# Optimization experiments

Measured on AMD Instinct MI355X. Metric: run time of the kernel, lower is better.

## Reference

```python
import jax, jax.numpy as jnp
import numpy as np


def setup_inputs() -> dict:
    key = jax.random.key(0)
    k1, k2, k3, k4 = jax.random.split(key, 4)
    B, S, I, O = 2, 4096, 4096, 4096
    x = jax.random.normal(k1, (B, S, I), dtype=jnp.float32)
    # packed int4 weights: each byte holds two nibbles; [O, I//2]
    qweight = jax.random.randint(k2, (O, I // 2), 0, 256, dtype=jnp.int32)
    # per-tensor weight scale (scalar, stored as shape [1])
    weight_scale = jax.random.uniform(k3, (1,), dtype=jnp.float32) * 0.01 + 1e-3
    bias = jax.random.normal(k4, (O,), dtype=jnp.float32)
    return {"x": x, "qweight": qweight, "weight_scale": weight_scale, "bias": bias}


def _dequant_weight(qweight, weight_scale):
    # unpack_int4 (dim=1): high nibble -> even cols, low nibble -> odd cols
    high = (qweight >> 4) - 8           # [O, I//2], values in [-8, 7]
    low = (qweight & 15) - 8            # [O, I//2]
    unpacked = jnp.stack([high, low], axis=-1).reshape(qweight.shape[0], -1)  # [O, I]
    # no weight_offset -> w = q * scale
    return unpacked.astype(weight_scale.dtype) * weight_scale


def reference(x, qweight, weight_scale, bias):
    w = _dequant_weight(qweight, weight_scale)  # [O, I] fp32
    # dynamic per-tensor symmetric int8 activation quantization
    max_abs = jnp.max(jnp.abs(x))
    scale = max_abs / 127.0
    scale = jnp.where(scale == 0, jnp.ones_like(scale), scale)
    x_dq = jnp.round(x / scale) * scale  # fake-quantized activations (offset = 0)
    # F.linear: x @ w.T + bias
    out = jnp.einsum('bsi,oi->bso', x_dq, w) + bias
    return out.astype(x.dtype)
```

## Files before the change

### kernel.cpp

```cpp
#include <hip/hip_runtime.h>


typedef __attribute__((ext_vector_type(4))) int int32x4;

__device__ __forceinline__ void async_copy16(const void* gsrc, void* ldsdst) {
  __builtin_amdgcn_global_load_lds(
      (const __attribute__((address_space(1))) void*)gsrc,
      (__attribute__((address_space(3))) void*)ldsdst, 16, 0, 0);
}

__global__ void amax_kernel(const float* __restrict__ x,
                            float* __restrict__ partial, int n4) {
  int tid = blockIdx.x * blockDim.x + threadIdx.x;
  int stride = gridDim.x * blockDim.x;
  float m = 0.0f;
  const float4* x4 = (const float4*)x;
  for (int i = tid; i < n4; i += stride) {
    float4 v = x4[i];
    m = fmaxf(m, fmaxf(fmaxf(fabsf(v.x), fabsf(v.y)),
                       fmaxf(fabsf(v.z), fabsf(v.w))));
  }
#pragma unroll
  for (int off = 32; off > 0; off >>= 1)
    m = fmaxf(m, __shfl_down(m, off, 64));
  __shared__ float red[4];
  if ((threadIdx.x & 63) == 0) red[threadIdx.x >> 6] = m;
  __syncthreads();
  if (threadIdx.x == 0) {
    partial[blockIdx.x] = fmaxf(fmaxf(red[0], red[1]), fmaxf(red[2], red[3]));
  }
}

__global__ void quant_kernel(const float* __restrict__ x,
                             const float* __restrict__ partial,
                             float* __restrict__ amax_out,
                             unsigned* __restrict__ qx, int n4) {
  const int t = threadIdx.x;
  float m = fmaxf(partial[t], partial[t + 256]);
#pragma unroll
  for (int off = 32; off > 0; off >>= 1)
    m = fmaxf(m, __shfl_down(m, off, 64));
  __shared__ float red[4];
  if ((t & 63) == 0) red[t >> 6] = m;
  __syncthreads();
  __shared__ float s_bcast;
  if (t == 0) {
    float amax = fmaxf(fmaxf(red[0], red[1]), fmaxf(red[2], red[3]));
    if (blockIdx.x == 0) *amax_out = amax;
    float s = amax / 127.0f;
    if (s == 0.0f) s = 1.0f;
    s_bcast = 1.0f / s;
  }
  __syncthreads();
  const float inv = s_bcast;

  int tid = blockIdx.x * blockDim.x + t;
  int stride = gridDim.x * blockDim.x;
  const float4* x4 = (const float4*)x;
  for (int i = tid; i < n4; i += stride) {
    float4 v = x4[i];
    int a = __float2int_rn(v.x * inv);
    int b = __float2int_rn(v.y * inv);
    int c = __float2int_rn(v.z * inv);
    int d = __float2int_rn(v.w * inv);
    qx[i] = (unsigned)(a & 0xFF) | ((unsigned)(b & 0xFF) << 8) |
            ((unsigned)(c & 0xFF) << 16) | ((unsigned)(d & 0xFF) << 24);
  }
}

__device__ __forceinline__ unsigned pack2(int q) {
  unsigned hi = (unsigned)((((q >> 4) & 15) - 8) & 0xFF);
  unsigned lo = (unsigned)(((q & 15) - 8) & 0xFF);
  return hi | (lo << 8);
}

__global__ void repack_kernel(const int* __restrict__ qw,
                              uint2* __restrict__ w8, int n4) {
  int tid = blockIdx.x * blockDim.x + threadIdx.x;
  int stride = gridDim.x * blockDim.x;
  const int4* q4 = (const int4*)qw;
  for (int i = tid; i < n4; i += stride) {
    int4 q = q4[i];
    uint2 r;
    r.x = pack2(q.x) | (pack2(q.y) << 16);
    r.y = pack2(q.z) | (pack2(q.w) << 16);
    w8[i] = r;
  }
}

#define BM 256
#define BN 256
#define BKT 64
#define TILE_B (BM * BKT)

#define TILE_BODY(t, CUR_AL, CUR_BF, NXT_AL, NXT_BF)                          \
  {                                                                           \
    const char* Ab = &As[((t) & 3) * TILE_B];                                 \
     \
    _Pragma("unroll") for (int i = 0; i < 4; ++i) afH[i] =                    \
        *(const int32x4*)(Ab + (arow0 + 64 + i * 16) * BKT + xsl);            \
    if ((t) + 3 < NT) {                                                       \
      const char* sa = aS + ((t) + 3) * BKT;                                  \
      char* ad = aD + (((t) + 3) & 3) * TILE_B;                               \
      async_copy16(sa, ad);                                                   \
      async_copy16(sa + skip, ad + 8192);                                     \
    }                                                                         \
     \
    asm volatile("s_waitcnt lgkmcnt(4)" ::: "memory");                        \
    __builtin_amdgcn_s_setprio(1);                                            \
    _Pragma("unroll") for (int i = 0; i < 4; ++i)                             \
        _Pragma("unroll") for (int j = 0; j < 4; ++j) acc[i][j] =             \
            __builtin_amdgcn_mfma_i32_16x16x64_i8(CUR_AL[i], CUR_BF[j],       \
                                                  acc[i][j], 0, 0, 0);        \
    __builtin_amdgcn_s_setprio(0);                                            \
           \
    if ((t) + 1 < NT) {                                                       \
           \
      asm volatile("s_waitcnt lgkmcnt(0)" ::: "memory");                      \
        \
      if ((t) + 4 <= NT)                                                      \
        asm volatile("s_waitcnt vmcnt(6)" ::: "memory");                      \
      else if ((t) + 3 <= NT)                                                 \
        asm volatile("s_waitcnt vmcnt(4)" ::: "memory");                      \
      else                                                                    \
        asm volatile("s_waitcnt vmcnt(0)" ::: "memory");                      \
      __builtin_amdgcn_s_barrier();                                           \
      __builtin_amdgcn_sched_barrier(0);    \
      const char* Abn = &As[(((t) + 1) & 3) * TILE_B];                        \
      const char* Bbn = &Bs[(((t) + 1) & 3) * TILE_B];                        \
      _Pragma("unroll") for (int i = 0; i < 4; ++i) NXT_AL[i] =               \
          *(const int32x4*)(Abn + (arow0 + i * 16) * BKT + xsl);              \
      _Pragma("unroll") for (int j = 0; j < 4; ++j) NXT_BF[j] =               \
          *(const int32x4*)(Bbn + (brow0 + j * 16) * BKT + xsl);              \
    }                                                                         \
    if ((t) + 3 < NT) {                                                       \
      const char* sb = bS + ((t) + 3) * BKT;                                  \
      char* bd = bD + (((t) + 3) & 3) * TILE_B;                               \
      async_copy16(sb, bd);                                                   \
      async_copy16(sb + skip, bd + 8192);                                     \
    }                                                                         \
    __builtin_amdgcn_s_setprio(1);                                            \
    _Pragma("unroll") for (int i = 0; i < 4; ++i)                             \
        _Pragma("unroll") for (int j = 0; j < 4; ++j) acc[4 + i][j] =         \
            __builtin_amdgcn_mfma_i32_16x16x64_i8(afH[i], CUR_BF[j],          \
                                                  acc[4 + i][j], 0, 0, 0);    \
    __builtin_amdgcn_s_setprio(0);                                            \
  }

__global__ __launch_bounds__(512, 2) void gemm_i8(
    const char* __restrict__ A, const char* __restrict__ Bt,
    const float* __restrict__ bias, const float* __restrict__ amax_p,
    const float* __restrict__ wscale, float* __restrict__ C,
    int M, int N, int K) {
  __shared__ alignas(16) char As[4 * TILE_B];
  __shared__ alignas(16) char Bs[4 * TILE_B];

  const int tid = threadIdx.x;
  const int lane = tid & 63;
  const int wave = tid >> 6;
  const int wm = wave >> 2;
  const int wn = wave & 3;
  const int quad = lane >> 4;
  const int l16 = lane & 15;

  const int cpx = gridDim.x >> 3;
  const int wg = (blockIdx.x & 7) * cpx + (blockIdx.x >> 3);
  const int bM = (wg >> 4) * BM;
  const int bN = (wg & 15) * BN;

  const int NT = K >> 6;

  const int srow = tid >> 2;
  const int scoff = (((tid & 3) ^ ((tid >> 3) & 3)) << 4);
  const char* aS = A + (size_t)(bM + srow) * K + scoff;
  const char* bS = Bt + (size_t)(bN + srow) * K + scoff;
  const size_t skip = (size_t)128 * K;
  char* aD = &As[tid * 16];
  char* bD = &Bs[tid * 16];

  for (int tt = 0; tt < 3; ++tt) {
    const int boff = tt * TILE_B;
    const char* sa = aS + tt * BKT;
    const char* sb = bS + tt * BKT;
    async_copy16(sa, aD + boff);
    async_copy16(sa + skip, aD + boff + 8192);
    async_copy16(sb, bD + boff);
    async_copy16(sb + skip, bD + boff + 8192);
  }

  const int xsl = ((quad ^ ((l16 >> 1) & 3)) << 4);
  const int arow0 = (wm << 7) + l16;
  const int brow0 = (wn << 6) + l16;

  int32x4 acc[8][4] = {};
  int32x4 afL0[4], bf0[4], afL1[4], bf1[4], afH[4];

  asm volatile("s_waitcnt vmcnt(8)" ::: "memory");
  __builtin_amdgcn_s_barrier();
  __builtin_amdgcn_sched_barrier(0);

#pragma unroll
  for (int i = 0; i < 4; ++i)
    afL0[i] = *(const int32x4*)(&As[0] + (arow0 + i * 16) * BKT + xsl);
#pragma unroll
  for (int j = 0; j < 4; ++j)
    bf0[j] = *(const int32x4*)(&Bs[0] + (brow0 + j * 16) * BKT + xsl);

  for (int t = 0; t < NT; t += 2) {
    TILE_BODY(t, afL0, bf0, afL1, bf1);
    TILE_BODY(t + 1, afL1, bf1, afL0, bf0);
  }

  float s = *amax_p / 127.0f;
  if (s == 0.0f) s = 1.0f;
  const float cs = s * wscale[0];

#pragma unroll
  for (int f = 0; f < 8; ++f) {
#pragma unroll
    for (int j = 0; j < 4; ++j) {
      const int n = bN + (wn << 6) + j * 16 + l16;
#pragma unroll
      for (int r = 0; r < 4; ++r) {
        const int m = bM + (wm << 7) + f * 16 + quad * 4 + r;
        C[(size_t)m * N + n] = (float)acc[f][j][r] * cs + bias[n];
      }
    }
  }
}

extern "C" void kernel_launch(void* const* d_in, const int* in_sizes, int n_in,
                              void* d_out, int out_size, void* d_ws,
                              size_t ws_size, hipStream_t stream) {
  const float* x = (const float*)d_in[0];
  const int* qw = (const int*)d_in[1];
  const float* wscale = (const float*)d_in[2];
  const float* bias = (const float*)d_in[3];
  float* out = (float*)d_out;

  const int nx = in_sizes[0];
  const int npacked = in_sizes[1];
  const int O = in_sizes[3];
  const int I = (npacked / O) * 2;
  const int M = nx / I;

  float* amax = (float*)d_ws;
  float* partial = (float*)((char*)d_ws + 256);
  char* qx = (char*)d_ws + 8192;
  char* w8 = qx + (size_t)nx;

  amax_kernel<<<512, 256, 0, stream>>>(x, partial, nx / 4);
  quant_kernel<<<2048, 256, 0, stream>>>(x, partial, amax, (unsigned*)qx,
                                         nx / 4);
  repack_kernel<<<1024, 256, 0, stream>>>(qw, (uint2*)w8, npacked / 4);

  const int nwg = (M / BM) * (O / BN);
  gemm_i8<<<nwg, 512, 0, stream>>>(qx, w8, bias, amax, wscale, out, M, O, I);
}
```

Before: 397.1 us.

## Use 4-wave GEMM workgroups with 128x128 per-wave tiles and widen amax reduction

The int8 GEMM workgroup drops from 8 waves to 4, and each wave now computes a 128x128 output tile (8x8 MFMA fragments) instead of 128x64. Each thread issues four async global-to-LDS copies per operand per stage instead of two, and the vmcnt thresholds are adjusted to match. The aim is more register-level reuse of A/B fragments per LDS read. The cost is a large jump in accumulator VGPR usage (256 accumulator registers), one workgroup per CU, and less latency hiding. Separately, the amax kernel gets twice as many blocks, each loop iteration loads two float4s, and the quant kernel reduces over 1024 partials.

```diff
diff --git a/kernel.cpp b/kernel.cpp
--- a/kernel.cpp
+++ b/kernel.cpp
@@ -15,10 +15,14 @@
   int stride = gridDim.x * blockDim.x;
   float m = 0.0f;
   const float4* x4 = (const float4*)x;
-  for (int i = tid; i < n4; i += stride) {
+  for (int i = tid; i < n4; i += 2 * stride) {
     float4 v = x4[i];
+    float4 w = (i + stride < n4) ? x4[i + stride]
+                                 : make_float4(0.f, 0.f, 0.f, 0.f);
     m = fmaxf(m, fmaxf(fmaxf(fabsf(v.x), fabsf(v.y)),
                        fmaxf(fabsf(v.z), fabsf(v.w))));
+    m = fmaxf(m, fmaxf(fmaxf(fabsf(w.x), fabsf(w.y)),
+                       fmaxf(fabsf(w.z), fabsf(w.w))));
   }
 #pragma unroll
   for (int off = 32; off > 0; off >>= 1)
@@ -36,7 +40,8 @@
                              float* __restrict__ amax_out,
                              unsigned* __restrict__ qx, int n4) {
   const int t = threadIdx.x;
-  float m = fmaxf(partial[t], partial[t + 256]);
+  float m = fmaxf(fmaxf(partial[t], partial[t + 256]),
+                  fmaxf(partial[t + 512], partial[t + 768]));
 #pragma unroll
   for (int off = 32; off > 0; off >>= 1)
     m = fmaxf(m, __shfl_down(m, off, 64));
@@ -96,32 +101,33 @@
 #define TILE_BODY(t, CUR_AL, CUR_BF, NXT_AL, NXT_BF)                          \
   {                                                                           \
     const char* Ab = &As[((t) & 3) * TILE_B];                                 \
-     \
+       \
     _Pragma("unroll") for (int i = 0; i < 4; ++i) afH[i] =                    \
         *(const int32x4*)(Ab + (arow0 + 64 + i * 16) * BKT + xsl);            \
     if ((t) + 3 < NT) {                                                       \
       const char* sa = aS + ((t) + 3) * BKT;                                  \
       char* ad = aD + (((t) + 3) & 3) * TILE_B;                               \
       async_copy16(sa, ad);                                                   \
-      async_copy16(sa + skip, ad + 8192);                                     \
+      async_copy16(sa + skip1, ad + 4096);                                    \
+      async_copy16(sa + skip2, ad + 8192);                                    \
+      async_copy16(sa + skip3, ad + 12288);                                   \
     }                                                                         \
-     \
+          \
     asm volatile("s_waitcnt lgkmcnt(4)" ::: "memory");                        \
     __builtin_amdgcn_s_setprio(1);                                            \
     _Pragma("unroll") for (int i = 0; i < 4; ++i)                             \
-        _Pragma("unroll") for (int j = 0; j < 4; ++j) acc[i][j] =             \
+        _Pragma("unroll") for (int j = 0; j < 8; ++j) acc[i][j] =             \
             __builtin_amdgcn_mfma_i32_16x16x64_i8(CUR_AL[i], CUR_BF[j],       \
                                                   acc[i][j], 0, 0, 0);        \
     __builtin_amdgcn_s_setprio(0);                                            \
            \
     if ((t) + 1 < NT) {                                                       \
-           \
       asm volatile("s_waitcnt lgkmcnt(0)" ::: "memory");                      \
-        \
+                   \
       if ((t) + 4 <= NT)                                                      \
-        asm volatile("s_waitcnt vmcnt(6)" ::: "memory");                      \
+        asm volatile("s_waitcnt vmcnt(12)" ::: "memory");                     \
       else if ((t) + 3 <= NT)                                                 \
-        asm volatile("s_waitcnt vmcnt(4)" ::: "memory");                      \
+        asm volatile("s_waitcnt vmcnt(8)" ::: "memory");                      \
       else                                                                    \
         asm volatile("s_waitcnt vmcnt(0)" ::: "memory");                      \
       __builtin_amdgcn_s_barrier();                                           \
@@ -130,24 +136,26 @@
       const char* Bbn = &Bs[(((t) + 1) & 3) * TILE_B];                        \
       _Pragma("unroll") for (int i = 0; i < 4; ++i) NXT_AL[i] =               \
           *(const int32x4*)(Abn + (arow0 + i * 16) * BKT + xsl);              \
-      _Pragma("unroll") for (int j = 0; j < 4; ++j) NXT_BF[j] =               \
+      _Pragma("unroll") for (int j = 0; j < 8; ++j) NXT_BF[j] =               \
           *(const int32x4*)(Bbn + (brow0 + j * 16) * BKT + xsl);              \
     }                                                                         \
     if ((t) + 3 < NT) {                                                       \
       const char* sb = bS + ((t) + 3) * BKT;                                  \
       char* bd = bD + (((t) + 3) & 3) * TILE_B;                               \
       async_copy16(sb, bd);                                                   \
-      async_copy16(sb + skip, bd + 8192);                                     \
+      async_copy16(sb + skip1, bd + 4096);                                    \
+      async_copy16(sb + skip2, bd + 8192);                                    \
+      async_copy16(sb + skip3, bd + 12288);                                   \
     }                                                                         \
     __builtin_amdgcn_s_setprio(1);                                            \
     _Pragma("unroll") for (int i = 0; i < 4; ++i)                             \
-        _Pragma("unroll") for (int j = 0; j < 4; ++j) acc[4 + i][j] =         \
+        _Pragma("unroll") for (int j = 0; j < 8; ++j) acc[4 + i][j] =         \
             __builtin_amdgcn_mfma_i32_16x16x64_i8(afH[i], CUR_BF[j],          \
                                                   acc[4 + i][j], 0, 0, 0);    \
     __builtin_amdgcn_s_setprio(0);                                            \
   }
 
-__global__ __launch_bounds__(512, 2) void gemm_i8(
+__global__ __launch_bounds__(256, 1) void gemm_i8(
     const char* __restrict__ A, const char* __restrict__ Bt,
     const float* __restrict__ bias, const float* __restrict__ amax_p,
     const float* __restrict__ wscale, float* __restrict__ C,
@@ -158,8 +166,8 @@
   const int tid = threadIdx.x;
   const int lane = tid & 63;
   const int wave = tid >> 6;
-  const int wm = wave >> 2;
-  const int wn = wave & 3;
+  const int wm = wave >> 1;
+  const int wn = wave & 1;
   const int quad = lane >> 4;
   const int l16 = lane & 15;
 
@@ -174,7 +182,9 @@
   const int scoff = (((tid & 3) ^ ((tid >> 3) & 3)) << 4);
   const char* aS = A + (size_t)(bM + srow) * K + scoff;
   const char* bS = Bt + (size_t)(bN + srow) * K + scoff;
-  const size_t skip = (size_t)128 * K;
+  const size_t skip1 = (size_t)64 * K;
+  const size_t skip2 = (size_t)128 * K;
+  const size_t skip3 = (size_t)192 * K;
   char* aD = &As[tid * 16];
   char* bD = &Bs[tid * 16];
 
@@ -183,19 +193,24 @@
     const char* sa = aS + tt * BKT;
     const char* sb = bS + tt * BKT;
     async_copy16(sa, aD + boff);
-    async_copy16(sa + skip, aD + boff + 8192);
+    async_copy16(sa + skip1, aD + boff + 4096);
+    async_copy16(sa + skip2, aD + boff + 8192);
+    async_copy16(sa + skip3, aD + boff + 12288);
     async_copy16(sb, bD + boff);
-    async_copy16(sb + skip, bD + boff + 8192);
+    async_copy16(sb + skip1, bD + boff + 4096);
+    async_copy16(sb + skip2, bD + boff + 8192);
+    async_copy16(sb + skip3, bD + boff + 12288);
   }
 
   const int xsl = ((quad ^ ((l16 >> 1) & 3)) << 4);
   const int arow0 = (wm << 7) + l16;
-  const int brow0 = (wn << 6) + l16;
-
-  int32x4 acc[8][4] = {};
-  int32x4 afL0[4], bf0[4], afL1[4], bf1[4], afH[4];
-
-  asm volatile("s_waitcnt vmcnt(8)" ::: "memory");
+  const int brow0 = (wn << 7) + l16;
+
+  int32x4 acc[8][8] = {};
+  int32x4 afL0[4], afL1[4], afH[4];
+  int32x4 bf0[8], bf1[8];
+
+  asm volatile("s_waitcnt vmcnt(16)" ::: "memory");
   __builtin_amdgcn_s_barrier();
   __builtin_amdgcn_sched_barrier(0);
 
@@ -203,7 +218,7 @@
   for (int i = 0; i < 4; ++i)
     afL0[i] = *(const int32x4*)(&As[0] + (arow0 + i * 16) * BKT + xsl);
 #pragma unroll
-  for (int j = 0; j < 4; ++j)
+  for (int j = 0; j < 8; ++j)
     bf0[j] = *(const int32x4*)(&Bs[0] + (brow0 + j * 16) * BKT + xsl);
 
   for (int t = 0; t < NT; t += 2) {
@@ -216,14 +231,14 @@
   const float cs = s * wscale[0];
 
 #pragma unroll
-  for (int f = 0; f < 8; ++f) {
-#pragma unroll
-    for (int j = 0; j < 4; ++j) {
-      const int n = bN + (wn << 6) + j * 16 + l16;
+  for (int fi = 0; fi < 8; ++fi) {
+#pragma unroll
+    for (int fj = 0; fj < 8; ++fj) {
+      const int n = bN + (wn << 7) + fj * 16 + l16;
 #pragma unroll
       for (int r = 0; r < 4; ++r) {
-        const int m = bM + (wm << 7) + f * 16 + quad * 4 + r;
-        C[(size_t)m * N + n] = (float)acc[f][j][r] * cs + bias[n];
+        const int m = bM + (wm << 7) + fi * 16 + quad * 4 + r;
+        C[(size_t)m * N + n] = (float)acc[fi][fj][r] * cs + bias[n];
       }
     }
   }
@@ -249,11 +264,11 @@
   char* qx = (char*)d_ws + 8192;
   char* w8 = qx + (size_t)nx;
 
-  amax_kernel<<<512, 256, 0, stream>>>(x, partial, nx / 4);
+  amax_kernel<<<1024, 256, 0, stream>>>(x, partial, nx / 4);
   quant_kernel<<<2048, 256, 0, stream>>>(x, partial, amax, (unsigned*)qx,
                                          nx / 4);
   repack_kernel<<<1024, 256, 0, stream>>>(qw, (uint2*)w8, npacked / 4);
 
   const int nwg = (M / BM) * (O / BN);
-  gemm_i8<<<nwg, 512, 0, stream>>>(qx, w8, bias, amax, wscale, out, M, O, I);
-}
+  gemm_i8<<<nwg, 256, 0, stream>>>(qx, w8, bias, amax, wscale, out, M, O, I);
+}
```

Result: slower. 548.7 us (+38.2%).

## Restructure int8 GEMM into 3-stage ping-pong pipeline with fine-grained A fragment loads

Applied to the files above, without the earlier changes.

The GEMM main loop changes from a 4-buffer LDS ring to a 3-buffer ring. It splits each K tile into four MFMA groups separated by workgroup barriers, and loads A fragments two rows at a time, interleaved with async global-to-LDS copies. This cuts register pressure and interleaves LDS reads with MFMA work, with launch bounds dropped to 1 workgroup per CU. Separately, the amax reduction now uses 1024 blocks with 2 loads per iteration, and the quant kernel reduces 1024 partials. The many extra barriers and the lower occupancy may add stalls, and the shallower prefetch reduces how much load latency is hidden.

```diff
diff --git a/kernel.cpp b/kernel.cpp
--- a/kernel.cpp
+++ b/kernel.cpp
@@ -15,10 +15,14 @@
   int stride = gridDim.x * blockDim.x;
   float m = 0.0f;
   const float4* x4 = (const float4*)x;
-  for (int i = tid; i < n4; i += stride) {
+  for (int i = tid; i < n4; i += 2 * stride) {
     float4 v = x4[i];
+    float4 w = (i + stride < n4) ? x4[i + stride]
+                                 : make_float4(0.f, 0.f, 0.f, 0.f);
     m = fmaxf(m, fmaxf(fmaxf(fabsf(v.x), fabsf(v.y)),
                        fmaxf(fabsf(v.z), fabsf(v.w))));
+    m = fmaxf(m, fmaxf(fmaxf(fabsf(w.x), fabsf(w.y)),
+                       fmaxf(fabsf(w.z), fabsf(w.w))));
   }
 #pragma unroll
   for (int off = 32; off > 0; off >>= 1)
@@ -36,7 +40,8 @@
                              float* __restrict__ amax_out,
                              unsigned* __restrict__ qx, int n4) {
   const int t = threadIdx.x;
-  float m = fmaxf(partial[t], partial[t + 256]);
+  float m = fmaxf(fmaxf(partial[t], partial[t + 256]),
+                  fmaxf(partial[t + 512], partial[t + 768]));
 #pragma unroll
   for (int off = 32; off > 0; off >>= 1)
     m = fmaxf(m, __shfl_down(m, off, 64));
@@ -93,67 +98,83 @@
 #define BKT 64
 #define TILE_B (BM * BKT)
 
-#define TILE_BODY(t, CUR_AL, CUR_BF, NXT_AL, NXT_BF)                          \
+#define MFMA8(R0, R1, X0, X1, BF)                                          \
+  _Pragma("unroll") for (int j = 0; j < 4; ++j) {                          \
+    acc[R0][j] = __builtin_amdgcn_mfma_i32_16x16x64_i8(X0, BF[j],          \
+                                                       acc[R0][j], 0, 0, 0); \
+    acc[R1][j] = __builtin_amdgcn_mfma_i32_16x16x64_i8(X1, BF[j],          \
+                                                       acc[R1][j], 0, 0, 0); \
+  }
+
+#define TILE4(T, BFC, BFN)                                                    \
   {                                                                           \
-    const char* Ab = &As[((t) & 3) * TILE_B];                                 \
-     \
-    _Pragma("unroll") for (int i = 0; i < 4; ++i) afH[i] =                    \
-        *(const int32x4*)(Ab + (arow0 + 64 + i * 16) * BKT + xsl);            \
-    if ((t) + 3 < NT) {                                                       \
-      const char* sa = aS + ((t) + 3) * BKT;                                  \
-      char* ad = aD + (((t) + 3) & 3) * TILE_B;                               \
+    const char* Ab = &As[((T) % 3) * TILE_B];                                 \
+    const bool st = (T) + 2 < NT;                                \
+                \
+    pB0 = *(const int32x4*)(Ab + (arow0 + 32) * BKT + xsl);                   \
+    pB1 = *(const int32x4*)(Ab + (arow0 + 48) * BKT + xsl);                   \
+    if (st) {                                                                 \
+      const char* sa = aS + ((T) + 2) * BKT;                                  \
+      char* ad = &As[(((T) + 2) % 3) * TILE_B] + tid * 16;                    \
       async_copy16(sa, ad);                                                   \
       async_copy16(sa + skip, ad + 8192);                                     \
     }                                                                         \
-     \
-    asm volatile("s_waitcnt lgkmcnt(4)" ::: "memory");                        \
-    __builtin_amdgcn_s_setprio(1);                                            \
-    _Pragma("unroll") for (int i = 0; i < 4; ++i)                             \
-        _Pragma("unroll") for (int j = 0; j < 4; ++j) acc[i][j] =             \
-            __builtin_amdgcn_mfma_i32_16x16x64_i8(CUR_AL[i], CUR_BF[j],       \
-                                                  acc[i][j], 0, 0, 0);        \
-    __builtin_amdgcn_s_setprio(0);                                            \
-           \
-    if ((t) + 1 < NT) {                                                       \
-           \
-      asm volatile("s_waitcnt lgkmcnt(0)" ::: "memory");                      \
-        \
-      if ((t) + 4 <= NT)                                                      \
-        asm volatile("s_waitcnt vmcnt(6)" ::: "memory");                      \
-      else if ((t) + 3 <= NT)                                                 \
-        asm volatile("s_waitcnt vmcnt(4)" ::: "memory");                      \
-      else                                                                    \
-        asm volatile("s_waitcnt vmcnt(0)" ::: "memory");                      \
-      __builtin_amdgcn_s_barrier();                                           \
-      __builtin_amdgcn_sched_barrier(0);    \
-      const char* Abn = &As[(((t) + 1) & 3) * TILE_B];                        \
-      const char* Bbn = &Bs[(((t) + 1) & 3) * TILE_B];                        \
-      _Pragma("unroll") for (int i = 0; i < 4; ++i) NXT_AL[i] =               \
-          *(const int32x4*)(Abn + (arow0 + i * 16) * BKT + xsl);              \
-      _Pragma("unroll") for (int j = 0; j < 4; ++j) NXT_BF[j] =               \
-          *(const int32x4*)(Bbn + (brow0 + j * 16) * BKT + xsl);              \
-    }                                                                         \
-    if ((t) + 3 < NT) {                                                       \
-      const char* sb = bS + ((t) + 3) * BKT;                                  \
-      char* bd = bD + (((t) + 3) & 3) * TILE_B;                               \
+    __builtin_amdgcn_s_barrier();                                             \
+    __builtin_amdgcn_s_setprio(1);                                            \
+    MFMA8(0, 1, pA0, pA1, BFC)                                                \
+    __builtin_amdgcn_s_setprio(0);                                            \
+    __builtin_amdgcn_s_barrier();                                             \
+                \
+    pA0 = *(const int32x4*)(Ab + (arow0 + 64) * BKT + xsl);                   \
+    pA1 = *(const int32x4*)(Ab + (arow0 + 80) * BKT + xsl);                   \
+    if (st) {                                                                 \
+      const char* sb = bS + ((T) + 2) * BKT;                                  \
+      char* bd = &Bs[(((T) + 2) % 3) * TILE_B] + tid * 16;                    \
       async_copy16(sb, bd);                                                   \
       async_copy16(sb + skip, bd + 8192);                                     \
     }                                                                         \
-    __builtin_amdgcn_s_setprio(1);                                            \
-    _Pragma("unroll") for (int i = 0; i < 4; ++i)                             \
-        _Pragma("unroll") for (int j = 0; j < 4; ++j) acc[4 + i][j] =         \
-            __builtin_amdgcn_mfma_i32_16x16x64_i8(afH[i], CUR_BF[j],          \
-                                                  acc[4 + i][j], 0, 0, 0);    \
-    __builtin_amdgcn_s_setprio(0);                                            \
-  }
-
-__global__ __launch_bounds__(512, 2) void gemm_i8(
+    __builtin_amdgcn_s_barrier();                                             \
+    __builtin_amdgcn_s_setprio(1);                                            \
+    MFMA8(2, 3, pB0, pB1, BFC)                                                \
+    __builtin_amdgcn_s_setprio(0);                                            \
+    __builtin_amdgcn_s_barrier();                                             \
+     \
+    pB0 = *(const int32x4*)(Ab + (arow0 + 96) * BKT + xsl);                   \
+    pB1 = *(const int32x4*)(Ab + (arow0 + 112) * BKT + xsl);                  \
+    __builtin_amdgcn_s_barrier();                                             \
+    __builtin_amdgcn_s_setprio(1);                                            \
+    MFMA8(4, 5, pA0, pA1, BFC)                                                \
+    __builtin_amdgcn_s_setprio(0);                                            \
+                 \
+    if (st)                                                                   \
+      asm volatile("s_waitcnt vmcnt(4)" ::: "memory");                        \
+    else                                                                      \
+      asm volatile("s_waitcnt vmcnt(0)" ::: "memory");                        \
+    __builtin_amdgcn_s_barrier();                                             \
+    __builtin_amdgcn_sched_barrier(0);        \
+               \
+    if ((T) + 1 < NT) {                                                       \
+      const char* Abn = &As[(((T) + 1) % 3) * TILE_B];                        \
+      const char* Bbn = &Bs[(((T) + 1) % 3) * TILE_B];                        \
+      pA0 = *(const int32x4*)(Abn + (arow0 + 0) * BKT + xsl);                 \
+      pA1 = *(const int32x4*)(Abn + (arow0 + 16) * BKT + xsl);                \
+      _Pragma("unroll") for (int j = 0; j < 4; ++j) BFN[j] =                  \
+          *(const int32x4*)(Bbn + (brow0 + j * 16) * BKT + xsl);              \
+    }                                                                         \
+    __builtin_amdgcn_s_barrier();                                             \
+    __builtin_amdgcn_s_setprio(1);                                            \
+    MFMA8(6, 7, pB0, pB1, BFC)                                                \
+    __builtin_amdgcn_s_setprio(0);                                            \
+    __builtin_amdgcn_s_barrier();                                             \
+  }
+
+__global__ __launch_bounds__(512, 1) void gemm_i8(
     const char* __restrict__ A, const char* __restrict__ Bt,
     const float* __restrict__ bias, const float* __restrict__ amax_p,
     const float* __restrict__ wscale, float* __restrict__ C,
     int M, int N, int K) {
-  __shared__ alignas(16) char As[4 * TILE_B];
-  __shared__ alignas(16) char Bs[4 * TILE_B];
+  __shared__ alignas(16) char As[3 * TILE_B];
+  __shared__ alignas(16) char Bs[3 * TILE_B];
 
   const int tid = threadIdx.x;
   const int lane = tid & 63;
@@ -175,17 +196,15 @@
   const char* aS = A + (size_t)(bM + srow) * K + scoff;
   const char* bS = Bt + (size_t)(bN + srow) * K + scoff;
   const size_t skip = (size_t)128 * K;
-  char* aD = &As[tid * 16];
-  char* bD = &Bs[tid * 16];
-
-  for (int tt = 0; tt < 3; ++tt) {
+
+  for (int tt = 0; tt < 2; ++tt) {
     const int boff = tt * TILE_B;
     const char* sa = aS + tt * BKT;
     const char* sb = bS + tt * BKT;
-    async_copy16(sa, aD + boff);
-    async_copy16(sa + skip, aD + boff + 8192);
-    async_copy16(sb, bD + boff);
-    async_copy16(sb + skip, bD + boff + 8192);
+    async_copy16(sa, &As[boff] + tid * 16);
+    async_copy16(sa + skip, &As[boff + 8192] + tid * 16);
+    async_copy16(sb, &Bs[boff] + tid * 16);
+    async_copy16(sb + skip, &Bs[boff + 8192] + tid * 16);
   }
 
   const int xsl = ((quad ^ ((l16 >> 1) & 3)) << 4);
@@ -193,22 +212,22 @@
   const int brow0 = (wn << 6) + l16;
 
   int32x4 acc[8][4] = {};
-  int32x4 afL0[4], bf0[4], afL1[4], bf1[4], afH[4];
-
-  asm volatile("s_waitcnt vmcnt(8)" ::: "memory");
+  int32x4 pA0, pA1, pB0, pB1;
+  int32x4 bfA[4], bfB[4];
+
+  asm volatile("s_waitcnt vmcnt(4)" ::: "memory");
   __builtin_amdgcn_s_barrier();
   __builtin_amdgcn_sched_barrier(0);
 
-#pragma unroll
-  for (int i = 0; i < 4; ++i)
-    afL0[i] = *(const int32x4*)(&As[0] + (arow0 + i * 16) * BKT + xsl);
+  pA0 = *(const int32x4*)(&As[0] + (arow0 + 0) * BKT + xsl);
+  pA1 = *(const int32x4*)(&As[0] + (arow0 + 16) * BKT + xsl);
 #pragma unroll
   for (int j = 0; j < 4; ++j)
-    bf0[j] = *(const int32x4*)(&Bs[0] + (brow0 + j * 16) * BKT + xsl);
+    bfA[j] = *(const int32x4*)(&Bs[0] + (brow0 + j * 16) * BKT + xsl);
 
   for (int t = 0; t < NT; t += 2) {
-    TILE_BODY(t, afL0, bf0, afL1, bf1);
-    TILE_BODY(t + 1, afL1, bf1, afL0, bf0);
+    TILE4(t, bfA, bfB);
+    TILE4(t + 1, bfB, bfA);
   }
 
   float s = *amax_p / 127.0f;
@@ -249,7 +268,7 @@
   char* qx = (char*)d_ws + 8192;
   char* w8 = qx + (size_t)nx;
 
-  amax_kernel<<<512, 256, 0, stream>>>(x, partial, nx / 4);
+  amax_kernel<<<1024, 256, 0, stream>>>(x, partial, nx / 4);
   quant_kernel<<<2048, 256, 0, stream>>>(x, partial, amax, (unsigned*)qx,
                                          nx / 4);
   repack_kernel<<<1024, 256, 0, stream>>>(qw, (uint2*)w8, npacked / 4);
```

Result: slower. 430.3 us (+8.4%).

## Fuse amax, quantize and weight repack into one cooperative kernel with grid sync

Applied to the files above, without the earlier changes.

Merges the three preprocessing kernels into a single cooperative launch. Each block computes its partial amax and repacks the int4 weights, then a grid-wide sync lets every block reduce the 1024 partials and quantize x. This removes two kernel launches and their inter-kernel gaps, and overlaps the weight repack with the amax pass. In exchange it relies on all 1024 blocks being co-resident for the grid sync, and adds the cost of that sync.

```diff
diff --git a/kernel.cpp b/kernel.cpp
--- a/kernel.cpp
+++ b/kernel.cpp
@@ -1,4 +1,7 @@
 #include <hip/hip_runtime.h>
+#include <hip/hip_cooperative_groups.h>
+
+namespace cg = cooperative_groups;
 
 
 typedef __attribute__((ext_vector_type(4))) int int32x4;
@@ -9,10 +12,22 @@
       (__attribute__((address_space(3))) void*)ldsdst, 16, 0, 0);
 }
 
-__global__ void amax_kernel(const float* __restrict__ x,
-                            float* __restrict__ partial, int n4) {
-  int tid = blockIdx.x * blockDim.x + threadIdx.x;
-  int stride = gridDim.x * blockDim.x;
+__device__ __forceinline__ unsigned pack2(int q) {
+  unsigned hi = (unsigned)((((q >> 4) & 15) - 8) & 0xFF);
+  unsigned lo = (unsigned)(((q & 15) - 8) & 0xFF);
+  return hi | (lo << 8);
+}
+
+__global__ void prep_kernel(const float* __restrict__ x,
+                            const int* __restrict__ qw,
+                            float* __restrict__ partial,
+                            float* __restrict__ amax_out,
+                            unsigned* __restrict__ qx,
+                            uint2* __restrict__ w8, int n4, int nq4) {
+  const int t = threadIdx.x;
+  const int tid = blockIdx.x * blockDim.x + t;
+  const int stride = gridDim.x * blockDim.x;
+
   float m = 0.0f;
   const float4* x4 = (const float4*)x;
   for (int i = tid; i < n4; i += stride) {
@@ -24,24 +39,30 @@
   for (int off = 32; off > 0; off >>= 1)
     m = fmaxf(m, __shfl_down(m, off, 64));
   __shared__ float red[4];
-  if ((threadIdx.x & 63) == 0) red[threadIdx.x >> 6] = m;
+  if ((t & 63) == 0) red[t >> 6] = m;
   __syncthreads();
-  if (threadIdx.x == 0) {
+  if (t == 0) {
     partial[blockIdx.x] = fmaxf(fmaxf(red[0], red[1]), fmaxf(red[2], red[3]));
   }
-}
-
-__global__ void quant_kernel(const float* __restrict__ x,
-                             const float* __restrict__ partial,
-                             float* __restrict__ amax_out,
-                             unsigned* __restrict__ qx, int n4) {
-  const int t = threadIdx.x;
-  float m = fmaxf(partial[t], partial[t + 256]);
+
+  const int4* q4 = (const int4*)qw;
+  for (int i = tid; i < nq4; i += stride) {
+    int4 q = q4[i];
+    uint2 r;
+    r.x = pack2(q.x) | (pack2(q.y) << 16);
+    r.y = pack2(q.z) | (pack2(q.w) << 16);
+    w8[i] = r;
+  }
+
+  __threadfence();
+  cg::this_grid().sync();
+
+  float mm = fmaxf(fmaxf(partial[t], partial[t + 256]),
+                   fmaxf(partial[t + 512], partial[t + 768]));
 #pragma unroll
   for (int off = 32; off > 0; off >>= 1)
-    m = fmaxf(m, __shfl_down(m, off, 64));
-  __shared__ float red[4];
-  if ((t & 63) == 0) red[t >> 6] = m;
+    mm = fmaxf(mm, __shfl_down(mm, off, 64));
+  if ((t & 63) == 0) red[t >> 6] = mm;
   __syncthreads();
   __shared__ float s_bcast;
   if (t == 0) {
@@ -54,9 +75,6 @@
   __syncthreads();
   const float inv = s_bcast;
 
-  int tid = blockIdx.x * blockDim.x + t;
-  int stride = gridDim.x * blockDim.x;
-  const float4* x4 = (const float4*)x;
   for (int i = tid; i < n4; i += stride) {
     float4 v = x4[i];
     int a = __float2int_rn(v.x * inv);
@@ -65,26 +83,6 @@
     int d = __float2int_rn(v.w * inv);
     qx[i] = (unsigned)(a & 0xFF) | ((unsigned)(b & 0xFF) << 8) |
             ((unsigned)(c & 0xFF) << 16) | ((unsigned)(d & 0xFF) << 24);
-  }
-}
-
-__device__ __forceinline__ unsigned pack2(int q) {
-  unsigned hi = (unsigned)((((q >> 4) & 15) - 8) & 0xFF);
-  unsigned lo = (unsigned)(((q & 15) - 8) & 0xFF);
-  return hi | (lo << 8);
-}
-
-__global__ void repack_kernel(const int* __restrict__ qw,
-                              uint2* __restrict__ w8, int n4) {
-  int tid = blockIdx.x * blockDim.x + threadIdx.x;
-  int stride = gridDim.x * blockDim.x;
-  const int4* q4 = (const int4*)qw;
-  for (int i = tid; i < n4; i += stride) {
-    int4 q = q4[i];
-    uint2 r;
-    r.x = pack2(q.x) | (pack2(q.y) << 16);
-    r.y = pack2(q.z) | (pack2(q.w) << 16);
-    w8[i] = r;
   }
 }
 
@@ -246,14 +244,18 @@
 
   float* amax = (float*)d_ws;
   float* partial = (float*)((char*)d_ws + 256);
-  char* qx = (char*)d_ws + 8192;
-  char* w8 = qx + (size_t)nx;
-
-  amax_kernel<<<512, 256, 0, stream>>>(x, partial, nx / 4);
-  quant_kernel<<<2048, 256, 0, stream>>>(x, partial, amax, (unsigned*)qx,
-                                         nx / 4);
-  repack_kernel<<<1024, 256, 0, stream>>>(qw, (uint2*)w8, npacked / 4);
+  unsigned* qx = (unsigned*)((char*)d_ws + 8192);
+  uint2* w8 = (uint2*)((char*)qx + (size_t)nx);
+
+  int n4 = nx / 4;
+  int nq4 = npacked / 4;
+
+  void* args[] = {(void*)&x,    (void*)&qw, (void*)&partial, (void*)&amax,
+                  (void*)&qx,   (void*)&w8, (void*)&n4,      (void*)&nq4};
+  hipLaunchCooperativeKernel((const void*)prep_kernel, dim3(1024), dim3(256),
+                             args, 0, stream);
 
   const int nwg = (M / BM) * (O / BN);
-  gemm_i8<<<nwg, 512, 0, stream>>>(qx, w8, bias, amax, wscale, out, M, O, I);
-}
+  gemm_i8<<<nwg, 512, 0, stream>>>((const char*)qx, (const char*)w8, bias,
+                                   amax, wscale, out, M, O, I);
+}
```

Measured after the change: 581.6 us. 1.46x slower.
